# Kernel tuning notes

Measured on AMD Instinct MI355X. Metric: run time of the kernel, lower is better.

## Reference

```python
import jax, jax.numpy as jnp
import numpy as np

N_ITEMS = 50000; LM_IN = 768; D = 128; B = 256; L = 50
NH = 2; NL = 2; FF = 4 * D
TEMP = 0.1; BETA1 = 0.5; BETA2 = 0.5
NEG = -1e9


def _ln(x, g, b, eps=1e-5):
    m = x.mean(-1, keepdims=True)
    v = ((x - m) ** 2).mean(-1, keepdims=True)
    return (x - m) / jnp.sqrt(v + eps) * g + b


def _encoder(h, mask, P):
    # SASRec/BERT-style TransformerEncoder: pos-emb + LN, then NL blocks of
    # causal+padding-masked MHA and GELU FFN with post-LN residuals.
    pos, ln0g, ln0b, Wqkv, bqkv, Wo, bo, l1g, l1b, W1, b1, W2, b2, l2g, l2b = P
    Bh, Lh, Dh = h.shape
    dh = Dh // NH
    keep = jnp.tril(jnp.broadcast_to((mask != 0)[:, None, None, :], (Bh, 1, Lh, Lh)))
    bias = jnp.where(keep, 0.0, NEG)  # additive attention mask, [B,1,L,L]
    h = _ln(h + pos, ln0g, ln0b)
    scale = float(1.0 / np.sqrt(dh))
    for l in range(NL):
        qkv = h @ Wqkv[l] + bqkv[l]
        q, k, v = jnp.split(qkv, 3, axis=-1)
        sp = lambda t: t.reshape(Bh, Lh, NH, dh).transpose(0, 2, 1, 3)
        q, k, v = sp(q), sp(k), sp(v)
        att = jax.nn.softmax(jnp.einsum('bhqd,bhkd->bhqk', q, k) * scale + bias, axis=-1)
        o = jnp.einsum('bhqk,bhkd->bhqd', att, v).transpose(0, 2, 1, 3).reshape(Bh, Lh, Dh)
        h = _ln(h + o @ Wo[l] + bo[l], l1g[l], l1b[l])
        f = jax.nn.gelu(h @ W1[l] + b1[l]) @ W2[l] + b2[l]
        h = _ln(h + f, l2g[l], l2b[l])
    return h


def _last(trans, mask):
    # gather embedding at the last valid position: index = mask.sum(1) - 1
    idx = mask.sum(1).astype(jnp.int32) - 1
    return jnp.take_along_axis(trans, idx[:, None, None], axis=1)[:, 0]


def setup_inputs():
    key = jax.random.key(0)
    ks = jax.random.split(key, 32)
    s = 0.02

    def p(i, shape):
        return jax.random.normal(ks[i], shape, jnp.float32) * s

    inp = {}
    inp['x'] = jax.random.normal(ks[0], (N_ITEMS, LM_IN), jnp.float32)
    inp['uid'] = jax.random.randint(ks[1], (B,), 0, 100000)
    inp['edge_index'] = jax.random.randint(ks[2], (2, 1000), 0, N_ITEMS)
    inp['max_itemid'] = N_ITEMS - 1
    inp['itemid'] = jax.random.randint(ks[3], (B, L), 0, N_ITEMS)
    inp['mask'] = jnp.ones((B, L), jnp.float32)
    inp['id_emb'] = p(4, (N_ITEMS, D))
    inp['id_ln_g'] = jnp.ones(D); inp['id_ln_b'] = jnp.zeros(D)
    inp['text_W'] = p(5, (LM_IN, D)); inp['text_b'] = jnp.zeros(D)
    inp['text_ln_g'] = jnp.ones(D); inp['text_ln_b'] = jnp.zeros(D)
    for pre, base in (('ide_', 6), ('te_', 16)):
        inp[pre + 'pos'] = p(base, (L, D))
        inp[pre + 'ln0_g'] = jnp.ones(D); inp[pre + 'ln0_b'] = jnp.zeros(D)
        inp[pre + 'Wqkv'] = p(base + 1, (NL, D, 3 * D)); inp[pre + 'bqkv'] = jnp.zeros((NL, 3 * D))
        inp[pre + 'Wo'] = p(base + 2, (NL, D, D)); inp[pre + 'bo'] = jnp.zeros((NL, D))
        inp[pre + 'ln1_g'] = jnp.ones((NL, D)); inp[pre + 'ln1_b'] = jnp.zeros((NL, D))
        inp[pre + 'W1'] = p(base + 3, (NL, D, FF)); inp[pre + 'b1'] = jnp.zeros((NL, FF))
        inp[pre + 'W2'] = p(base + 4, (NL, FF, D)); inp[pre + 'b2'] = jnp.zeros((NL, D))
        inp[pre + 'ln2_g'] = jnp.ones((NL, D)); inp[pre + 'ln2_b'] = jnp.zeros((NL, D))
    return inp


def reference(x, uid, edge_index, max_itemid, itemid, mask,
              id_emb, id_ln_g, id_ln_b, text_W, text_b, text_ln_g, text_ln_b,
              ide_pos, ide_ln0_g, ide_ln0_b, ide_Wqkv, ide_bqkv, ide_Wo, ide_bo,
              ide_ln1_g, ide_ln1_b, ide_W1, ide_b1, ide_W2, ide_b2, ide_ln2_g, ide_ln2_b,
              te_pos, te_ln0_g, te_ln0_b, te_Wqkv, te_bqkv, te_Wo, te_bo,
              te_ln1_g, te_ln1_b, te_W1, te_b1, te_W2, te_b2, te_ln2_g, te_ln2_b):
    # --- ID module: layernorm over the full embedding table, gather, encode ---
    gnn_emb = _ln(id_emb, id_ln_g, id_ln_b)  # [n_items, D]
    ideP = (ide_pos, ide_ln0_g, ide_ln0_b, ide_Wqkv, ide_bqkv, ide_Wo, ide_bo,
            ide_ln1_g, ide_ln1_b, ide_W1, ide_b1, ide_W2, ide_b2, ide_ln2_g, ide_ln2_b)
    trans = _encoder(gnn_emb[itemid], mask, ideP)  # [B,L,D]
    session_emb = _last(trans, mask)  # [B,D]
    item_embs = gnn_emb[:max_itemid + 1]
    scores1 = session_emb @ item_embs.T  # [B, n_items]
    # --- Text module: linear+relu (dropout off at eval), layernorm, encode ---
    xmap = _ln(jax.nn.relu(x @ text_W + text_b), text_ln_g, text_ln_b)  # [n_items, D]
    teP = (te_pos, te_ln0_g, te_ln0_b, te_Wqkv, te_bqkv, te_Wo, te_bo,
           te_ln1_g, te_ln1_b, te_W1, te_b1, te_W2, te_b2, te_ln2_g, te_ln2_b)
    trans2 = _encoder(xmap[itemid], mask, teP)
    session_feat = _last(trans2, mask)
    scores2 = (session_feat @ xmap[:max_itemid + 1].T) / TEMP
    # eval path: combined score
    scores = BETA1 * scores1 + BETA2 * scores2
    return (scores, scores1, scores2, item_embs, gnn_emb[:max_itemid + 1], xmap[:max_itemid + 1])
```

## Files before the change

### kernel.cpp

```cpp
#include <hip/hip_runtime.h>

#define DEV __device__ __forceinline__

typedef float f32x4 __attribute__((ext_vector_type(4)));
typedef __bf16 bf16x8 __attribute__((ext_vector_type(8)));
#define MFMA16(a,b,c) __builtin_amdgcn_mfma_f32_16x16x32_bf16(a,b,c,0,0,0)

#define LSTRIDE 132
#define ASTRIDE 136
#define QSTRIDE 72

DEV float wsum(float v){
  #pragma unroll
  for (int o = 32; o > 0; o >>= 1) v += __shfl_xor(v, o, 64);
  return v;
}

DEV float gelu_f(float x){
  float u = 0.7978845608028654f * (x + 0.044715f * x * x * x);
  float e = __expf(2.f * u);
  float th = 1.f - 2.f / (e + 1.f);
  return 0.5f * x * (1.f + th);
}

__global__ __launch_bounds__(256) void ln_kernel(const float* in,
    float* out0, float* out1,
    const float* __restrict__ g, const float* __restrict__ bb, int nrows)
{
  int w = threadIdx.x >> 6, l = threadIdx.x & 63;
  int row = blockIdx.x * 4 + w;
  if (row >= nrows) return;
  const float* rp = in + (size_t)row * 128;
  float v0 = rp[l], v1 = rp[l + 64];
  float m = wsum(v0 + v1) * 0.0078125f;
  float d0 = v0 - m, d1 = v1 - m;
  float var = wsum(d0 * d0 + d1 * d1) * 0.0078125f;
  float rs = rsqrtf(var + 1e-5f);
  float o0 = d0 * rs * g[l] + bb[l];
  float o1 = d1 * rs * g[l + 64] + bb[l + 64];
  size_t base = (size_t)row * 128;
  out0[base + l] = o0; out0[base + l + 64] = o1;
  if (out1){ out1[base + l] = o0; out1[base + l + 64] = o1; }
}

__global__ __launch_bounds__(256) void prep_w(
    const float* __restrict__ Wa, const float* __restrict__ Wb,
    __bf16* __restrict__ dst, int K, int N, int nmat)
{
  int tid = blockIdx.x * 256 + threadIdx.x;
  int tpm = (N >> 4) * (K >> 5);
  if (tid >= nmat * tpm * 64) return;
  int lane = tid & 63;
  int tile = (tid >> 6) % tpm;
  int mat  = tid / (tpm * 64);
  const float* W;
  if (nmat == 1) W = Wa;
  else W = ((mat >> 1) ? Wb : Wa) + (size_t)(mat & 1) * K * N;
  int kdiv = K >> 5;
  int nt = tile / kdiv, kt = tile - nt * kdiv;
  int col  = nt * 16 + (lane & 15);
  int krow = kt * 32 + (lane >> 4) * 8;
  __bf16 v[8];
  #pragma unroll
  for (int j = 0; j < 8; j++) v[j] = (__bf16)W[(size_t)(krow + j) * N + col];
  *(bf16x8*)(dst + (size_t)tid * 8) = *(bf16x8*)v;
}

__global__ __launch_bounds__(256) void xmap_mfma(
    const float* __restrict__ X, const __bf16* __restrict__ wt,
    const float* __restrict__ bias, float* __restrict__ out)
{
  __shared__ __bf16 xb[64 * ASTRIDE];
  const int t = threadIdx.x, w = t >> 6, l = t & 63, lm = l & 15, quad = l >> 4;
  const int r0 = blockIdx.x * 64;
  f32x4 acc[8];
  #pragma unroll
  for (int nt = 0; nt < 8; nt++) acc[nt] = (f32x4){0.f,0.f,0.f,0.f};
  for (int kc = 0; kc < 6; kc++){
    for (int i = t; i < 64 * 32; i += 256){
      int r = i >> 5, c4 = (i & 31) * 4;
      float4 v = make_float4(0.f,0.f,0.f,0.f);
      if (r0 + r < 50000) v = *(const float4*)&X[(size_t)(r0 + r) * 768 + kc * 128 + c4];
      xb[r*ASTRIDE + c4 + 0] = (__bf16)v.x;
      xb[r*ASTRIDE + c4 + 1] = (__bf16)v.y;
      xb[r*ASTRIDE + c4 + 2] = (__bf16)v.z;
      xb[r*ASTRIDE + c4 + 3] = (__bf16)v.w;
    }
    __syncthreads();
    bf16x8 af[4];
    #pragma unroll
    for (int kt = 0; kt < 4; kt++)
      af[kt] = *(const bf16x8*)&xb[(w*16 + lm)*ASTRIDE + kt*32 + quad*8];
    #pragma unroll
    for (int nt = 0; nt < 8; nt++)
      #pragma unroll
      for (int kt = 0; kt < 4; kt++)
        acc[nt] = MFMA16(af[kt], *(const bf16x8*)(wt + ((size_t)(nt*24 + kc*4 + kt)*64 + l)*8), acc[nt]);
    __syncthreads();
  }
  #pragma unroll
  for (int nt = 0; nt < 8; nt++){
    int n = nt*16 + lm;
    float bs = bias[n];
    #pragma unroll
    for (int r = 0; r < 4; r++){
      int row = r0 + w*16 + quad*4 + r;
      if (row < 50000) out[(size_t)row*128 + n] = fmaxf(acc[nt][r] + bs, 0.f);
    }
  }
}

struct EncP {
  const float *pos, *ln0g, *ln0b, *bqkv, *bo, *ln1g, *ln1b, *b1, *b2, *ln2g, *ln2b;
  const __bf16 *wq, *wo, *w1, *w2;
  const float* emb;
  float* outT;
};

DEV void ln_rows(float* hb, const float* g, const float* bb, int w, int l){
  for (int r = w; r < 50; r += 4){
    float v0 = hb[r*LSTRIDE + l], v1 = hb[r*LSTRIDE + l + 64];
    float m = wsum(v0 + v1) * 0.0078125f;
    float d0 = v0 - m, d1 = v1 - m;
    float var = wsum(d0*d0 + d1*d1) * 0.0078125f;
    float rs = rsqrtf(var + 1e-5f);
    hb[r*LSTRIDE + l]      = d0 * rs * g[l] + bb[l];
    hb[r*LSTRIDE + l + 64] = d1 * rs * g[l + 64] + bb[l + 64];
  }
}

__global__ __launch_bounds__(256) void encoder_mfma(
    EncP P0, EncP P1, const int* __restrict__ itemid, const float* __restrict__ mask)
{
  EncP P = (blockIdx.x < 256) ? P0 : P1;
  const int b = blockIdx.x & 255;
  const int t = threadIdx.x, w = t >> 6, l = t & 63;
  const int lm = l & 15, quad = l >> 4;
  const int mb = w * 16;
  const int am = mb + lm;

  __shared__ float  hf[50 * LSTRIDE];
  __shared__ __bf16 ab[64 * ASTRIDE];
  __shared__ __bf16 qkbuf[2 * 64 * QSTRIDE];
  __shared__ __bf16 vb[64 * QSTRIDE];
  __shared__ float  maskv[64];

  if (t < 64) maskv[t] = (t < 50) ? mask[b*50 + t] : 0.f;

  for (int r = w; r < 50; r += 4){
    int it = itemid[b*50 + r];
    const float* er = P.emb + (size_t)it * 128;
    float v0 = er[l]      + P.pos[r*128 + l];
    float v1 = er[l + 64] + P.pos[r*128 + l + 64];
    float m = wsum(v0 + v1) * 0.0078125f;
    float d0 = v0 - m, d1 = v1 - m;
    float var = wsum(d0*d0 + d1*d1) * 0.0078125f;
    float rs = rsqrtf(var + 1e-5f);
    hf[r*LSTRIDE + l]      = d0 * rs * P.ln0g[l] + P.ln0b[l];
    hf[r*LSTRIDE + l + 64] = d1 * rs * P.ln0g[l + 64] + P.ln0b[l + 64];
  }
  __syncthreads();

  for (int lay = 0; lay < 2; ++lay){
    const __bf16* wq = P.wq + lay * 49152;
    const __bf16* wo = P.wo + lay * 16384;
    const __bf16* w1 = P.w1 + lay * 65536;
    const __bf16* w2 = P.w2 + lay * 65536;
    const float* bq  = P.bqkv + lay * 384;
    const float* bo  = P.bo   + lay * 128;
    const float* g1  = P.ln1g + lay * 128;
    const float* b1n = P.ln1b + lay * 128;
    const float* b1f = P.b1   + lay * 512;
    const float* b2f = P.b2   + lay * 128;
    const float* g2  = P.ln2g + lay * 128;
    const float* b2n = P.ln2b + lay * 128;

    for (int i = t; i < 64 * 128; i += 256){
      int r = i >> 7, c = i & 127;
      ab[r*ASTRIDE + c] = (__bf16)((r < 50) ? hf[r*LSTRIDE + c] : 0.f);
    }
    __syncthreads();

    bf16x8 afh[4];
    #pragma unroll
    for (int kt = 0; kt < 4; kt++)
      afh[kt] = *(const bf16x8*)&ab[am*ASTRIDE + kt*32 + quad*8];

    for (int hd = 0; hd < 2; hd++){
      if (hd) __syncthreads();
      __bf16* qb = qkbuf;
      __bf16* kb = qkbuf + 64*QSTRIDE;

      #pragma unroll
      for (int part = 0; part < 3; part++){
        #pragma unroll
        for (int tt = 0; tt < 4; tt++){
          int nt = part*8 + hd*4 + tt;
          f32x4 acc = (f32x4){0.f,0.f,0.f,0.f};
          #pragma unroll
          for (int kt = 0; kt < 4; kt++)
            acc = MFMA16(afh[kt], *(const bf16x8*)(wq + ((size_t)(nt*4 + kt)*64 + l)*8), acc);
          int n = nt*16 + lm;
          float bias = bq[n];
          int d = n & 63;
          #pragma unroll
          for (int r = 0; r < 4; r++){
            int m = mb + quad*4 + r;
            float v = acc[r] + bias;
            if (part == 0)      qb[m*QSTRIDE + d] = (__bf16)v;
            else if (part == 1) kb[m*QSTRIDE + d] = (__bf16)v;
            else                vb[d*QSTRIDE + m] = (__bf16)v;
          }
        }
      }
      __syncthreads();

      bf16x8 aq0 = *(const bf16x8*)&qb[am*QSTRIDE + quad*8];
      bf16x8 aq1 = *(const bf16x8*)&qb[am*QSTRIDE + 32 + quad*8];
      f32x4 sf[4];
      #pragma unroll
      for (int nt = 0; nt < 4; nt++){
        f32x4 acc = (f32x4){0.f,0.f,0.f,0.f};
        acc = MFMA16(aq0, *(const bf16x8*)&kb[(nt*16 + lm)*QSTRIDE + quad*8], acc);
        acc = MFMA16(aq1, *(const bf16x8*)&kb[(nt*16 + lm)*QSTRIDE + 32 + quad*8], acc);
        sf[nt] = acc;
      }
      #pragma unroll
      for (int r = 0; r < 4; r++){
        int q = mb + quad*4 + r;
        float sv[4];
        float mx = -3e38f;
        #pragma unroll
        for (int nt = 0; nt < 4; nt++){
          int ki = nt*16 + lm;
          float s = sf[nt][r] * 0.125f;
          bool keep = (ki <= q) && (maskv[ki] != 0.f);
          s = keep ? s : -1e9f;
          sv[nt] = s; mx = fmaxf(mx, s);
        }
        #pragma unroll
        for (int o = 1; o < 16; o <<= 1) mx = fmaxf(mx, __shfl_xor(mx, o, 64));
        float sum = 0.f;
        #pragma unroll
        for (int nt = 0; nt < 4; nt++){ float p = __expf(sv[nt] - mx); sv[nt] = p; sum += p; }
        #pragma unroll
        for (int o = 1; o < 16; o <<= 1) sum += __shfl_xor(sum, o, 64);
        float inv = 1.f / sum;
        #pragma unroll
        for (int nt = 0; nt < 4; nt++)
          qb[q*QSTRIDE + nt*16 + lm] = (__bf16)(sv[nt] * inv);
      }
      bf16x8 ap0 = *(const bf16x8*)&qb[am*QSTRIDE + quad*8];
      bf16x8 ap1 = *(const bf16x8*)&qb[am*QSTRIDE + 32 + quad*8];
      #pragma unroll
      for (int nt = 0; nt < 4; nt++){
        f32x4 acc = (f32x4){0.f,0.f,0.f,0.f};
        acc = MFMA16(ap0, *(const bf16x8*)&vb[(nt*16 + lm)*QSTRIDE + quad*8], acc);
        acc = MFMA16(ap1, *(const bf16x8*)&vb[(nt*16 + lm)*QSTRIDE + 32 + quad*8], acc);
        int dcol = hd*64 + nt*16 + lm;
        #pragma unroll
        for (int r = 0; r < 4; r++)
          ab[(mb + quad*4 + r)*ASTRIDE + dcol] = (__bf16)acc[r];
      }
    }

    {
      bf16x8 af[4];
      #pragma unroll
      for (int kt = 0; kt < 4; kt++)
        af[kt] = *(const bf16x8*)&ab[am*ASTRIDE + kt*32 + quad*8];
      #pragma unroll
      for (int nt = 0; nt < 8; nt++){
        f32x4 acc = (f32x4){0.f,0.f,0.f,0.f};
        #pragma unroll
        for (int kt = 0; kt < 4; kt++)
          acc = MFMA16(af[kt], *(const bf16x8*)(wo + ((size_t)(nt*4 + kt)*64 + l)*8), acc);
        int n = nt*16 + lm;
        float bias = bo[n];
        #pragma unroll
        for (int r = 0; r < 4; r++){
          int m = mb + quad*4 + r;
          if (m < 50) hf[m*LSTRIDE + n] += acc[r] + bias;
        }
      }
    }
    __syncthreads();
    ln_rows(hf, g1, b1n, w, l);
    __syncthreads();

    for (int i = t; i < 64 * 128; i += 256){
      int r = i >> 7, c = i & 127;
      ab[r*ASTRIDE + c] = (__bf16)((r < 50) ? hf[r*LSTRIDE + c] : 0.f);
    }
    __syncthreads();

    {
      bf16x8 ah[4];
      #pragma unroll
      for (int kt = 0; kt < 4; kt++)
        ah[kt] = *(const bf16x8*)&ab[am*ASTRIDE + kt*32 + quad*8];
      f32x4 acc2[8];
      #pragma unroll
      for (int nt = 0; nt < 8; nt++) acc2[nt] = (f32x4){0.f,0.f,0.f,0.f};
      __bf16* ab2 = qkbuf;
      for (int ch = 0; ch < 4; ch++){
        #pragma unroll
        for (int nt = 0; nt < 8; nt++){
          f32x4 acc = (f32x4){0.f,0.f,0.f,0.f};
          #pragma unroll
          for (int kt = 0; kt < 4; kt++)
            acc = MFMA16(ah[kt], *(const bf16x8*)(w1 + ((size_t)((ch*8 + nt)*4 + kt)*64 + l)*8), acc);
          int n = ch*128 + nt*16 + lm;
          float bias = b1f[n];
          #pragma unroll
          for (int r = 0; r < 4; r++)
            ab2[(mb + quad*4 + r)*ASTRIDE + nt*16 + lm] = (__bf16)gelu_f(acc[r] + bias);
        }
        bf16x8 a2[4];
        #pragma unroll
        for (int kt = 0; kt < 4; kt++)
          a2[kt] = *(const bf16x8*)&ab2[am*ASTRIDE + kt*32 + quad*8];
        #pragma unroll
        for (int nt = 0; nt < 8; nt++)
          #pragma unroll
          for (int kt = 0; kt < 4; kt++)
            acc2[nt] = MFMA16(a2[kt], *(const bf16x8*)(w2 + ((size_t)(nt*16 + ch*4 + kt)*64 + l)*8), acc2[nt]);
      }
      #pragma unroll
      for (int nt = 0; nt < 8; nt++){
        int n = nt*16 + lm;
        float bias = b2f[n];
        #pragma unroll
        for (int r = 0; r < 4; r++){
          int m = mb + quad*4 + r;
          if (m < 50) hf[m*LSTRIDE + n] += acc2[nt][r] + bias;
        }
      }
    }
    __syncthreads();
    ln_rows(hf, g2, b2n, w, l);
    __syncthreads();
  }

  if (t < 128){
    float sm = 0.f;
    for (int i = 0; i < 50; i++) sm += maskv[i];
    int idx = min(49, max(0, (int)sm - 1));
    P.outT[t*256 + b] = hf[idx*LSTRIDE + t];
  }
}

__global__ __launch_bounds__(256) void scores_kernel(
    const float* __restrict__ seT, const float* __restrict__ sfT,
    const float* __restrict__ ie,  const float* __restrict__ xm,
    float* __restrict__ sc, float* __restrict__ s1, float* __restrict__ s2)
{
  __shared__ float iet[16 * 128];
  __shared__ float xmt[16 * 128];
  const int t = threadIdx.x;
  const size_t j0 = (size_t)blockIdx.x * 16;
  {
    const float4* ig = (const float4*)(ie + j0 * 128);
    const float4* xg = (const float4*)(xm + j0 * 128);
    float4* a = (float4*)iet; float4* c4 = (float4*)xmt;
    for (int i = t; i < 512; i += 256){ a[i] = ig[i]; c4[i] = xg[i]; }
  }
  __syncthreads();
  float a1[16], a2[16];
  #pragma unroll
  for (int j = 0; j < 16; j++){ a1[j] = 0.f; a2[j] = 0.f; }
  for (int k = 0; k < 128; k += 4){
    float se0 = seT[(k+0)*256 + t], se1 = seT[(k+1)*256 + t];
    float se2 = seT[(k+2)*256 + t], se3 = seT[(k+3)*256 + t];
    float sf0 = sfT[(k+0)*256 + t], sf1 = sfT[(k+1)*256 + t];
    float sf2 = sfT[(k+2)*256 + t], sf3 = sfT[(k+3)*256 + t];
    #pragma unroll
    for (int j = 0; j < 16; j++){
      float4 iv = *(const float4*)&iet[j*128 + k];
      float4 xv = *(const float4*)&xmt[j*128 + k];
      a1[j] += iv.x*se0 + iv.y*se1 + iv.z*se2 + iv.w*se3;
      a2[j] += xv.x*sf0 + xv.y*sf1 + xv.z*sf2 + xv.w*sf3;
    }
  }
  size_t rb = (size_t)t * 50000 + j0;
  #pragma unroll
  for (int j = 0; j < 16; j += 4){
    float4 v1 = make_float4(a1[j], a1[j+1], a1[j+2], a1[j+3]);
    float4 v2 = make_float4(a2[j]*10.f, a2[j+1]*10.f, a2[j+2]*10.f, a2[j+3]*10.f);
    float4 vs = make_float4(0.5f*(v1.x+v2.x), 0.5f*(v1.y+v2.y),
                            0.5f*(v1.z+v2.z), 0.5f*(v1.w+v2.w));
    *(float4*)&s1[rb + j] = v1;
    *(float4*)&s2[rb + j] = v2;
    *(float4*)&sc[rb + j] = vs;
  }
}

extern "C" void kernel_launch(void* const* d_in, const int* in_sizes, int n_in,
                              void* d_out, int out_size, void* d_ws, size_t ws_size,
                              hipStream_t stream)
{
  const float* x       = (const float*)d_in[0];
  const int*   itemid  = (const int*)d_in[4];
  const float* mask    = (const float*)d_in[5];
  const float* id_emb  = (const float*)d_in[6];
  const float* id_g    = (const float*)d_in[7];
  const float* id_b    = (const float*)d_in[8];
  const float* text_W  = (const float*)d_in[9];
  const float* text_b  = (const float*)d_in[10];
  const float* text_g  = (const float*)d_in[11];
  const float* text_bb = (const float*)d_in[12];

  float* out = (float*)d_out;
  float* o_scores = out;
  float* o_s1     = out + 12800000;
  float* o_s2     = out + 25600000;
  float* o_item   = out + 38400000;
  float* o_gnn    = out + 44800000;
  float* o_xmap   = out + 51200000;

  float* seT = (float*)d_ws;
  float* sfT = seT + 32768;
  __bf16* wp   = (__bf16*)((char*)d_ws + 262144);
  __bf16* wqkv = wp;
  __bf16* wo   = wp + 196608;
  __bf16* w1p  = wp + 262144;
  __bf16* w2p  = wp + 524288;
  __bf16* wtx  = wp + 786432;

  prep_w<<<96, 256, 0, stream>>>((const float*)d_in[16], (const float*)d_in[31], wqkv, 128, 384, 4);
  prep_w<<<32, 256, 0, stream>>>((const float*)d_in[18], (const float*)d_in[33], wo,   128, 128, 4);
  prep_w<<<128,256, 0, stream>>>((const float*)d_in[22], (const float*)d_in[37], w1p,  128, 512, 4);
  prep_w<<<128,256, 0, stream>>>((const float*)d_in[24], (const float*)d_in[39], w2p,  512, 128, 4);
  prep_w<<<48, 256, 0, stream>>>(text_W, text_W, wtx, 768, 128, 1);

  ln_kernel<<<12500, 256, 0, stream>>>(id_emb, o_item, o_gnn, id_g, id_b, 50000);
  xmap_mfma<<<782, 256, 0, stream>>>(x, wtx, text_b, o_xmap);
  ln_kernel<<<12500, 256, 0, stream>>>(o_xmap, o_xmap, nullptr, text_g, text_bb, 50000);

  EncP P0, P1;
  P0.pos = (const float*)d_in[13]; P0.ln0g = (const float*)d_in[14]; P0.ln0b = (const float*)d_in[15];
  P0.bqkv = (const float*)d_in[17]; P0.bo = (const float*)d_in[19];
  P0.ln1g = (const float*)d_in[20]; P0.ln1b = (const float*)d_in[21];
  P0.b1 = (const float*)d_in[23]; P0.b2 = (const float*)d_in[25];
  P0.ln2g = (const float*)d_in[26]; P0.ln2b = (const float*)d_in[27];
  P0.wq = wqkv; P0.wo = wo; P0.w1 = w1p; P0.w2 = w2p;
  P0.emb = o_item; P0.outT = seT;

  P1.pos = (const float*)d_in[28]; P1.ln0g = (const float*)d_in[29]; P1.ln0b = (const float*)d_in[30];
  P1.bqkv = (const float*)d_in[32]; P1.bo = (const float*)d_in[34];
  P1.ln1g = (const float*)d_in[35]; P1.ln1b = (const float*)d_in[36];
  P1.b1 = (const float*)d_in[38]; P1.b2 = (const float*)d_in[40];
  P1.ln2g = (const float*)d_in[41]; P1.ln2b = (const float*)d_in[42];
  P1.wq = wqkv + 2*49152; P1.wo = wo + 2*16384; P1.w1 = w1p + 2*65536; P1.w2 = w2p + 2*65536;
  P1.emb = o_xmap; P1.outT = sfT;

  encoder_mfma<<<512, 256, 0, stream>>>(P0, P1, itemid, mask);

  scores_kernel<<<3125, 256, 0, stream>>>(seT, sfT, o_item, o_xmap,
                                          o_scores, o_s1, o_s2);
}
```

Baseline: 886.3 us.

## Keep encoder residual stream in registers and shrink shared memory pool

The fp32 residual activations move from a shared-memory buffer into per-lane registers laid out like the MFMA accumulators, and layernorm becomes a register-level reduction using 16-lane shuffles. Shared buffers are packed into one aliased pool, with Q and the softmax probabilities placed in the upper half of the activation buffer. This drops several block-wide syncs and shared round trips per layer. The launch bounds now ask for 4 blocks per CU, which may force register spilling given the 32-float residual array per thread.

```diff
diff --git a/kernel.cpp b/kernel.cpp
--- a/kernel.cpp
+++ b/kernel.cpp
@@ -6,9 +6,9 @@
 typedef __bf16 bf16x8 __attribute__((ext_vector_type(8)));
 #define MFMA16(a,b,c) __builtin_amdgcn_mfma_f32_16x16x32_bf16(a,b,c,0,0,0)
 
-#define LSTRIDE 132
 #define ASTRIDE 136
 #define QSTRIDE 72
+#define PSTRIDE 132
 
 DEV float wsum(float v){
   #pragma unroll
@@ -117,19 +117,41 @@
   float* outT;
 };
 
-DEV void ln_rows(float* hb, const float* g, const float* bb, int w, int l){
-  for (int r = w; r < 50; r += 4){
-    float v0 = hb[r*LSTRIDE + l], v1 = hb[r*LSTRIDE + l + 64];
-    float m = wsum(v0 + v1) * 0.0078125f;
-    float d0 = v0 - m, d1 = v1 - m;
-    float var = wsum(d0*d0 + d1*d1) * 0.0078125f;
-    float rs = rsqrtf(var + 1e-5f);
-    hb[r*LSTRIDE + l]      = d0 * rs * g[l] + bb[l];
-    hb[r*LSTRIDE + l + 64] = d1 * rs * g[l + 64] + bb[l + 64];
-  }
-}
-
-__global__ __launch_bounds__(256) void encoder_mfma(
+DEV void ln_reg(float res[8][4], const float* g, const float* bb, int lm){
+  float gv[8], bv[8];
+  #pragma unroll
+  for (int nt = 0; nt < 8; nt++){ gv[nt] = g[nt*16 + lm]; bv[nt] = bb[nt*16 + lm]; }
+  #pragma unroll
+  for (int r = 0; r < 4; r++){
+    float s = 0.f;
+    #pragma unroll
+    for (int nt = 0; nt < 8; nt++) s += res[nt][r];
+    s += __shfl_xor(s, 1, 64); s += __shfl_xor(s, 2, 64);
+    s += __shfl_xor(s, 4, 64); s += __shfl_xor(s, 8, 64);
+    float mean = s * 0.0078125f;
+    float v = 0.f;
+    #pragma unroll
+    for (int nt = 0; nt < 8; nt++){ float d = res[nt][r] - mean; v += d * d; }
+    v += __shfl_xor(v, 1, 64); v += __shfl_xor(v, 2, 64);
+    v += __shfl_xor(v, 4, 64); v += __shfl_xor(v, 8, 64);
+    float rs = rsqrtf(v * 0.0078125f + 1e-5f);
+    #pragma unroll
+    for (int nt = 0; nt < 8; nt++)
+      res[nt][r] = (res[nt][r] - mean) * rs * gv[nt] + bv[nt];
+  }
+}
+
+DEV void stage_res(const float res[8][4], __bf16* ab, int mb, int quad, int lm){
+  #pragma unroll
+  for (int r = 0; r < 4; r++){
+    int m = mb + quad*4 + r;
+    #pragma unroll
+    for (int nt = 0; nt < 8; nt++)
+      ab[m*ASTRIDE + nt*16 + lm] = (__bf16)res[nt][r];
+  }
+}
+
+__global__ __launch_bounds__(256, 4) void encoder_mfma(
     EncP P0, EncP P1, const int* __restrict__ itemid, const float* __restrict__ mask)
 {
   EncP P = (blockIdx.x < 256) ? P0 : P1;
@@ -139,11 +161,12 @@
   const int mb = w * 16;
   const int am = mb + lm;
 
-  __shared__ float  hf[50 * LSTRIDE];
-  __shared__ __bf16 ab[64 * ASTRIDE];
-  __shared__ __bf16 qkbuf[2 * 64 * QSTRIDE];
-  __shared__ __bf16 vb[64 * QSTRIDE];
-  __shared__ float  maskv[64];
+  __shared__ __align__(16) char pool[35840];
+  __bf16* ab = (__bf16*)pool;
+  __bf16* kb = (__bf16*)(pool + 17408);
+  __bf16* vb = (__bf16*)(pool + 17408 + 9216);
+  float*  hfp = (float*)pool;
+  __shared__ float maskv[64];
 
   if (t < 64) maskv[t] = (t < 50) ? mask[b*50 + t] : 0.f;
 
@@ -156,8 +179,18 @@
     float d0 = v0 - m, d1 = v1 - m;
     float var = wsum(d0*d0 + d1*d1) * 0.0078125f;
     float rs = rsqrtf(var + 1e-5f);
-    hf[r*LSTRIDE + l]      = d0 * rs * P.ln0g[l] + P.ln0b[l];
-    hf[r*LSTRIDE + l + 64] = d1 * rs * P.ln0g[l + 64] + P.ln0b[l + 64];
+    hfp[r*PSTRIDE + l]      = d0 * rs * P.ln0g[l] + P.ln0b[l];
+    hfp[r*PSTRIDE + l + 64] = d1 * rs * P.ln0g[l + 64] + P.ln0b[l + 64];
+  }
+  __syncthreads();
+
+  float res[8][4];
+  #pragma unroll
+  for (int r = 0; r < 4; r++){
+    int m = mb + quad*4 + r;
+    #pragma unroll
+    for (int nt = 0; nt < 8; nt++)
+      res[nt][r] = (m < 50) ? hfp[m*PSTRIDE + nt*16 + lm] : 0.f;
   }
   __syncthreads();
 
@@ -175,21 +208,14 @@
     const float* g2  = P.ln2g + lay * 128;
     const float* b2n = P.ln2b + lay * 128;
 
-    for (int i = t; i < 64 * 128; i += 256){
-      int r = i >> 7, c = i & 127;
-      ab[r*ASTRIDE + c] = (__bf16)((r < 50) ? hf[r*LSTRIDE + c] : 0.f);
-    }
-    __syncthreads();
-
+    stage_res(res, ab, mb, quad, lm);
     bf16x8 afh[4];
     #pragma unroll
     for (int kt = 0; kt < 4; kt++)
       afh[kt] = *(const bf16x8*)&ab[am*ASTRIDE + kt*32 + quad*8];
 
     for (int hd = 0; hd < 2; hd++){
-      if (hd) __syncthreads();
-      __bf16* qb = qkbuf;
-      __bf16* kb = qkbuf + 64*QSTRIDE;
+      __syncthreads();
 
       #pragma unroll
       for (int part = 0; part < 3; part++){
@@ -207,7 +233,7 @@
           for (int r = 0; r < 4; r++){
             int m = mb + quad*4 + r;
             float v = acc[r] + bias;
-            if (part == 0)      qb[m*QSTRIDE + d] = (__bf16)v;
+            if (part == 0)      ab[m*ASTRIDE + 64 + d] = (__bf16)v;
             else if (part == 1) kb[m*QSTRIDE + d] = (__bf16)v;
             else                vb[d*QSTRIDE + m] = (__bf16)v;
           }
@@ -215,8 +241,8 @@
       }
       __syncthreads();
 
-      bf16x8 aq0 = *(const bf16x8*)&qb[am*QSTRIDE + quad*8];
-      bf16x8 aq1 = *(const bf16x8*)&qb[am*QSTRIDE + 32 + quad*8];
+      bf16x8 aq0 = *(const bf16x8*)&ab[am*ASTRIDE + 64 + quad*8];
+      bf16x8 aq1 = *(const bf16x8*)&ab[am*ASTRIDE + 96 + quad*8];
       f32x4 sf[4];
       #pragma unroll
       for (int nt = 0; nt < 4; nt++){
@@ -248,10 +274,10 @@
         float inv = 1.f / sum;
         #pragma unroll
         for (int nt = 0; nt < 4; nt++)
-          qb[q*QSTRIDE + nt*16 + lm] = (__bf16)(sv[nt] * inv);
-      }
-      bf16x8 ap0 = *(const bf16x8*)&qb[am*QSTRIDE + quad*8];
-      bf16x8 ap1 = *(const bf16x8*)&qb[am*QSTRIDE + 32 + quad*8];
+          ab[q*ASTRIDE + 64 + nt*16 + lm] = (__bf16)(sv[nt] * inv);
+      }
+      bf16x8 ap0 = *(const bf16x8*)&ab[am*ASTRIDE + 64 + quad*8];
+      bf16x8 ap1 = *(const bf16x8*)&ab[am*ASTRIDE + 96 + quad*8];
       #pragma unroll
       for (int nt = 0; nt < 4; nt++){
         f32x4 acc = (f32x4){0.f,0.f,0.f,0.f};
@@ -275,25 +301,15 @@
         #pragma unroll
         for (int kt = 0; kt < 4; kt++)
           acc = MFMA16(af[kt], *(const bf16x8*)(wo + ((size_t)(nt*4 + kt)*64 + l)*8), acc);
-        int n = nt*16 + lm;
-        float bias = bo[n];
-        #pragma unroll
-        for (int r = 0; r < 4; r++){
-          int m = mb + quad*4 + r;
-          if (m < 50) hf[m*LSTRIDE + n] += acc[r] + bias;
-        }
-      }
-    }
-    __syncthreads();
-    ln_rows(hf, g1, b1n, w, l);
-    __syncthreads();
-
-    for (int i = t; i < 64 * 128; i += 256){
-      int r = i >> 7, c = i & 127;
-      ab[r*ASTRIDE + c] = (__bf16)((r < 50) ? hf[r*LSTRIDE + c] : 0.f);
-    }
-    __syncthreads();
-
+        float bias = bo[nt*16 + lm];
+        #pragma unroll
+        for (int r = 0; r < 4; r++)
+          res[nt][r] += acc[r] + bias;
+      }
+    }
+    ln_reg(res, g1, b1n, lm);
+
+    stage_res(res, ab, mb, quad, lm);
     {
       bf16x8 ah[4];
       #pragma unroll
@@ -302,7 +318,6 @@
       f32x4 acc2[8];
       #pragma unroll
       for (int nt = 0; nt < 8; nt++) acc2[nt] = (f32x4){0.f,0.f,0.f,0.f};
-      __bf16* ab2 = qkbuf;
       for (int ch = 0; ch < 4; ch++){
         #pragma unroll
         for (int nt = 0; nt < 8; nt++){
@@ -310,16 +325,15 @@
           #pragma unroll
           for (int kt = 0; kt < 4; kt++)
             acc = MFMA16(ah[kt], *(const bf16x8*)(w1 + ((size_t)((ch*8 + nt)*4 + kt)*64 + l)*8), acc);
-          int n = ch*128 + nt*16 + lm;
-          float bias = b1f[n];
+          float bias = b1f[ch*128 + nt*16 + lm];
           #pragma unroll
           for (int r = 0; r < 4; r++)
-            ab2[(mb + quad*4 + r)*ASTRIDE + nt*16 + lm] = (__bf16)gelu_f(acc[r] + bias);
+            ab[(mb + quad*4 + r)*ASTRIDE + nt*16 + lm] = (__bf16)gelu_f(acc[r] + bias);
         }
         bf16x8 a2[4];
         #pragma unroll
         for (int kt = 0; kt < 4; kt++)
-          a2[kt] = *(const bf16x8*)&ab2[am*ASTRIDE + kt*32 + quad*8];
+          a2[kt] = *(const bf16x8*)&ab[am*ASTRIDE + kt*32 + quad*8];
         #pragma unroll
         for (int nt = 0; nt < 8; nt++)
           #pragma unroll
@@ -328,25 +342,27 @@
       }
       #pragma unroll
       for (int nt = 0; nt < 8; nt++){
-        int n = nt*16 + lm;
-        float bias = b2f[n];
-        #pragma unroll
-        for (int r = 0; r < 4; r++){
-          int m = mb + quad*4 + r;
-          if (m < 50) hf[m*LSTRIDE + n] += acc2[nt][r] + bias;
-        }
-      }
-    }
-    __syncthreads();
-    ln_rows(hf, g2, b2n, w, l);
-    __syncthreads();
-  }
-
-  if (t < 128){
+        float bias = b2f[nt*16 + lm];
+        #pragma unroll
+        for (int r = 0; r < 4; r++)
+          res[nt][r] += acc2[nt][r] + bias;
+      }
+    }
+    ln_reg(res, g2, b2n, lm);
+  }
+
+  {
     float sm = 0.f;
     for (int i = 0; i < 50; i++) sm += maskv[i];
     int idx = min(49, max(0, (int)sm - 1));
-    P.outT[t*256 + b] = hf[idx*LSTRIDE + t];
+    #pragma unroll
+    for (int r = 0; r < 4; r++){
+      if (mb + quad*4 + r == idx){
+        #pragma unroll
+        for (int nt = 0; nt < 8; nt++)
+          P.outT[(nt*16 + lm)*256 + b] = res[nt][r];
+      }
+    }
   }
 }
 
```

Result: slower. 904.8 us (+2.1%).
